# Kernel tuning notes

Hardware: AMD Instinct MI355X
Metric: run time of the kernel (lower is better)

Reference implementation:

```python
import jax, jax.numpy as jnp
import numpy as np

B, N, F_IN, T = 4, 512, 64, 16
K, F_CHEB, F_TIME, TS = 3, 64, 64, 1
E = 16384
LN_EPS = 1e-5


def setup_inputs() -> dict:
    key = jax.random.key(0)
    ks = jax.random.split(key, 18)
    s = 0.05
    X = jax.random.normal(ks[0], (B, N, F_IN, T), jnp.float32)
    # edges with guaranteed no self-loops (so remove_self_loops is a no-op)
    src = jax.random.randint(ks[1], (E,), 0, N, jnp.int32)
    off = jax.random.randint(ks[2], (E,), 1, N, jnp.int32)
    dst = (src + off) % N
    edge_index = jnp.stack([src, dst])
    return {
        'X': X,
        'edge_index': edge_index,
        'U1': jax.random.uniform(ks[3], (N,)) * s,
        'U2': jax.random.normal(ks[4], (F_IN, N)) * s,
        'U3': jax.random.uniform(ks[5], (F_IN,)) * s,
        'be': jax.random.normal(ks[6], (1, T, T)) * s,
        'Ve': jax.random.normal(ks[7], (T, T)) * s,
        'Ws1': jax.random.uniform(ks[8], (T,)) * s,
        'Ws2': jax.random.normal(ks[9], (F_IN, T)) * s,
        'Ws3': jax.random.uniform(ks[10], (F_IN,)) * s,
        'bs': jax.random.normal(ks[11], (1, N, N)) * s,
        'Vs': jax.random.normal(ks[12], (N, N)) * s,
        'W_cheb': jax.random.normal(ks[13], (K, F_IN, F_CHEB)) * s,
        'b_cheb': jax.random.uniform(ks[14], (F_CHEB,)) * s,
        'Wt': jax.random.normal(ks[15], (F_TIME, F_CHEB, 1, 3)) * s,
        'bt': jnp.zeros((F_TIME,), jnp.float32),
        'Wr': jax.random.normal(ks[16], (F_TIME, F_IN, 1, 1)) * s,
        'br': jnp.zeros((F_TIME,), jnp.float32),
        'gamma': jnp.ones((F_TIME,), jnp.float32),
        'beta': jnp.zeros((F_TIME,), jnp.float32),
    }


def _forward(edge_index, X, U1, U2, U3, be, Ve, Ws1, Ws2, Ws3, bs, Vs,
             W_cheb, b_cheb, Wt, bt, Wr, br, gamma, beta):
    Bn, Nn, Fn, Tn = X.shape
    # ---- temporal attention: (B,T,T)
    lhs_t = jnp.einsum('bnft,n->btf', X, U1) @ U2            # (B,T,N)
    rhs_t = jnp.einsum('f,bnft->bnt', U3, X)                 # (B,N,T)
    Et = jnp.matmul(Ve, jax.nn.sigmoid(jnp.matmul(lhs_t, rhs_t) + be))
    Et = jax.nn.softmax(Et, axis=1)
    # temporally re-weighted signal
    Xt = jnp.matmul(X.reshape(Bn, Nn * Fn, Tn), Et).reshape(Bn, Nn, Fn, Tn)
    # ---- spatial attention: (B,N,N)
    lhs_s = jnp.einsum('bnft,t->bnf', Xt, Ws1) @ Ws2         # (B,N,T)
    rhs_s = jnp.einsum('f,bnft->btn', Ws3, Xt)               # (B,T,N)
    S = jnp.matmul(Vs, jax.nn.sigmoid(jnp.matmul(lhs_s, rhs_s) + bs))
    S = jax.nn.softmax(S, axis=1)                            # (B,N,N)
    # ---- scaled sym-normalized Laplacian; lambda_max=2 so 2/lambda_max = 1.
    # edges: -D^-1/2 A D^-1/2 (E), +I self loops (N), then add_self_loops(-1) (N)
    row, col = edge_index[0], edge_index[1]
    ew = jnp.ones(row.shape, X.dtype)
    deg = jnp.zeros((Nn,), X.dtype).at[row].add(ew)
    dis = jnp.where(deg > 0, 1.0 / jnp.sqrt(jnp.maximum(deg, 1.0)), 0.0)  # deg is integral so max() only guards deg==0
    wn = -dis[row] * dis[col]
    loops = jnp.arange(Nn)
    rows = jnp.concatenate([row, loops, loops])
    cols = jnp.concatenate([col, loops, loops])
    norm = jnp.concatenate([wn, jnp.ones((Nn,), X.dtype), -jnp.ones((Nn,), X.dtype)])
    att_norm = norm[None, :] * S[:, rows, cols]              # (B,Etot)

    def prop(h, w):
        # propagate over transposed edges: gather at col, scatter-add at row
        # h: (B,T,N,F); w broadcastable to (B,1,Etot)
        msg = w[..., None] * h[:, :, cols, :]
        return jnp.zeros_like(h).at[:, :, rows, :].add(msg)

    xt = X.transpose(0, 3, 1, 2)                             # (B,T,N,F): ChebConv applied per timestep
    Tx0 = jnp.diagonal(S, axis1=1, axis2=2)[:, None, :, None] * xt  # diag(S) @ x
    out = jnp.einsum('btnf,fg->btng', Tx0, W_cheb[0])
    if W_cheb.shape[0] > 1:
        Tx1 = prop(Tx0, att_norm[:, None, :])
        out = out + jnp.einsum('btnf,fg->btng', Tx1, W_cheb[1])
    for k in range(2, W_cheb.shape[0]):
        Tx2 = 2.0 * prop(Tx1, norm[None, None, :]) - Tx0
        out = out + jnp.einsum('btnf,fg->btng', Tx2, W_cheb[k])
        Tx0, Tx1 = Tx1, Tx2
    X_hat = jax.nn.relu(out + b_cheb)                        # (B,T,N,Fc)
    # ---- time conv (1x3, stride (1,TS)) on (B,Fc,N,T) + residual 1x1 conv
    conv_t = jax.lax.conv_general_dilated(
        X_hat.transpose(0, 3, 2, 1), Wt, (1, TS), ((0, 0), (1, 1)),
        dimension_numbers=('NCHW', 'OIHW', 'NCHW')) + bt[None, :, None, None]
    conv_r = jax.lax.conv_general_dilated(
        X.transpose(0, 2, 1, 3), Wr, (1, TS), ((0, 0), (0, 0)),
        dimension_numbers=('NCHW', 'OIHW', 'NCHW')) + br[None, :, None, None]
    Z = jax.nn.relu(conv_r + conv_t).transpose(0, 3, 2, 1)   # (B,T,N,Ft)
    mu = jnp.mean(Z, -1, keepdims=True)
    var = jnp.var(Z, -1, keepdims=True)
    Z = (Z - mu) / jnp.sqrt(var + LN_EPS) * gamma + beta     # LayerNorm over Ft
    return Z.transpose(0, 2, 3, 1)                           # (B,N,Ft,T)


def reference(X, edge_index, U1, U2, U3, be, Ve, Ws1, Ws2, Ws3, bs, Vs,
              W_cheb, b_cheb, Wt, bt, Wr, br, gamma, beta):
    return _forward(edge_index, X, U1, U2, U3, be, Ve, Ws1, Ws2, Ws3, bs, Vs,
                    W_cheb, b_cheb, Wt, bt, Wr, br, gamma, beta)
```

## Files before the change

### kernel.cpp

```cpp
#include <hip/hip_runtime.h>
#include <math.h>

#define NB 4
#define NV 512
#define NF 64
#define NT 16
#define NE 16384

#define TX1_OFF    2097152u
#define SIGT_OFF   4194304u
#define XHAT_OFF   6291456u
#define ST_OFF     TX1_OFF
#define BST_OFF    8388608u
#define ET_OFF     8650752u
#define PART_OFF   8651776u
#define RHST_OFF   8684544u
#define LHSS_OFF   8717312u
#define RHSSN_OFF  8750080u
#define DIAGS_OFF  8782848u
#define CSRW_OFF   8850432u
#define WTT_OFF    8866816u
#define WRT_OFF    8879104u
#define RHS3_OFF   8883712u
#define EW1_OFF    8916480u
#define MPART_OFF  8916544u
#define FEND       8949312u

__global__ void k_prep(const int* __restrict__ ei, int* __restrict__ counts,
                       const float* __restrict__ Wt, const float* __restrict__ Wr,
                       const float* __restrict__ bs,
                       float* __restrict__ WtT, float* __restrict__ WrT,
                       float* __restrict__ bsT,
                       const float* __restrict__ X, const float* __restrict__ U1,
                       const float* __restrict__ U3, const float* __restrict__ Ws3,
                       float* __restrict__ part, float* __restrict__ rhs,
                       float* __restrict__ rhs3) {
    __shared__ int h[512];
    __shared__ float tile[64][65];
    int bid = blockIdx.x, tid = threadIdx.x;
    if (bid < 64) {
        int c = bid;
        h[tid] = 0; h[tid + 256] = 0;
        __syncthreads();
        atomicAdd(&h[ei[c * 256 + tid]], 1);
        __syncthreads();
        counts[c * 512 + tid] = h[tid];
        counts[c * 512 + tid + 256] = h[tid + 256];
    } else if (bid < 128) {
        int tb = bid - 64;
        int r0 = (tb >> 3) * 64, c0 = (tb & 7) * 64;
        int c = tid & 63, rq = tid >> 6;
        for (int k = 0; k < 16; ++k) {
            int r = rq * 16 + k;
            tile[r][c] = bs[(r0 + r) * 512 + c0 + c];
        }
        __syncthreads();
        int r2 = tid & 63;
        for (int k = 0; k < 16; ++k) {
            int c2 = rq * 16 + k;
            bsT[(size_t)(c0 + c2) * 512 + r0 + r2] = tile[r2][c2];
        }
    } else if (bid < 192) {
        int idx = (bid - 128) * 256 + tid;
        if (idx < 12288) {
            int o = idx & 63, gd = idx >> 6;
            int g = gd / 3, dt = gd - g * 3;
            WtT[idx] = Wt[(o * 64 + g) * 3 + dt];
        } else {
            int i2 = idx - 12288;
            int o = i2 & 63, f = i2 >> 6;
            WrT[i2] = Wr[o * 64 + f];
        }
    } else {
        int sub = bid - 192;
        if (sub < 32) {
            int b = sub >> 3, g = sub & 7;
            float acc[4] = {0.f, 0.f, 0.f, 0.f};
            const float* Xb = X + (size_t)b * NV * 1024;
            int n0 = g * 64;
            for (int nn = 0; nn < 64; ++nn) {
                int n = n0 + nn;
                float u = U1[n];
                const float* xp = Xb + (size_t)n * 1024;
#pragma unroll
                for (int k = 0; k < 4; ++k) acc[k] += xp[tid + 256 * k] * u;
            }
#pragma unroll
            for (int k = 0; k < 4; ++k) part[(size_t)(b * 8 + g) * 1024 + tid + 256 * k] = acc[k];
        } else {
            int gid = (sub - 32) * 256 + tid;
            int t = gid & 15;
            const float* xp = X + ((size_t)(gid >> 4)) * 1024 + t;
            float a = 0.f, a3 = 0.f;
#pragma unroll
            for (int f = 0; f < 64; ++f) {
                float v = xp[f * 16];
                a += U3[f] * v;
                a3 += Ws3[f] * v;
            }
            rhs[gid] = a;
            rhs3[gid] = a3;
        }
    }
}

__global__ __launch_bounds__(512) void k_fillscan(const int* __restrict__ ei,
                                                  const int* __restrict__ counts,
                                                  int* __restrict__ row_start,
                                                  int* __restrict__ csr_col,
                                                  float* __restrict__ csr_w) {
    __shared__ int sc[512];
    __shared__ int base_l[512];
    __shared__ float dis_l[512];
    __shared__ int rs_l[512];
    __shared__ int rowL[256];
    int c = blockIdx.x, tid = threadIdx.x;
    int r = tid;
    int sum = 0, base = 0;
    for (int cc = 0; cc < 64; ++cc) {
        if (cc == c) base = sum;
        sum += counts[cc * 512 + r];
    }
    base_l[r] = base;
    dis_l[r] = sum > 0 ? 1.0f / sqrtf((float)sum) : 0.0f;
    sc[r] = sum;
    __syncthreads();
    for (int off = 1; off < 512; off <<= 1) {
        int v = sc[r];
        int add = (r >= off) ? sc[r - off] : 0;
        __syncthreads();
        sc[r] = v + add;
        __syncthreads();
    }
    rs_l[r] = sc[r] - sum;
    if (c == 0) {
        row_start[r] = sc[r] - sum;
        if (r == 511) row_start[512] = sc[r];
    }
    if (tid < 256) rowL[tid] = ei[c * 256 + tid];
    __syncthreads();
    if (tid < 256) {
        int rr = rowL[tid];
        int col = ei[NE + c * 256 + tid];
        int rank = 0;
        for (int j = 0; j < tid; ++j)
            if (rowL[j] == rr) rank++;
        int pos = rs_l[rr] + base_l[rr] + rank;
        csr_col[pos] = col;
        csr_w[pos] = -dis_l[rr] * dis_l[col];
    }
}

__global__ void k_mpart(const float* __restrict__ rhs_g, const float* __restrict__ U2,
                        float* __restrict__ Mpart) {
    __shared__ float rhsL[1024];
    int b = blockIdx.x >> 3, g = blockIdx.x & 7;
    int tid = threadIdx.x;
#pragma unroll
    for (int k = 0; k < 4; ++k)
        rhsL[tid + 256 * k] = rhs_g[(size_t)b * 8192 + g * 1024 + tid + 256 * k];
    __syncthreads();
    float acc[4] = {0.f, 0.f, 0.f, 0.f};
    int fA[4], tA[4];
#pragma unroll
    for (int k = 0; k < 4; ++k) { int idx = tid + 256 * k; fA[k] = idx >> 4; tA[k] = idx & 15; }
    int n0 = g * 64;
    for (int nn = 0; nn < 64; ++nn) {
#pragma unroll
        for (int k = 0; k < 4; ++k)
            acc[k] += U2[fA[k] * 512 + n0 + nn] * rhsL[nn * 16 + tA[k]];
    }
#pragma unroll
    for (int k = 0; k < 4; ++k) Mpart[(size_t)(b * 8 + g) * 1024 + tid + 256 * k] = acc[k];
}

__global__ void k_temporal(const float* __restrict__ part, const float* __restrict__ Mpart,
                           const float* __restrict__ be,
                           const float* __restrict__ Ve, const float* __restrict__ Ws1,
                           float* __restrict__ Et, float* __restrict__ ew1) {
    __shared__ float lhs1[1024];
    __shared__ float M[1024];
    __shared__ float Esig[256];
    __shared__ float Et0[256];
    __shared__ float red[32];
    __shared__ float EtL[256];
    int b = blockIdx.x, tid = threadIdx.x;
#pragma unroll
    for (int k = 0; k < 4; ++k) {
        int idx = tid + 256 * k;
        float s = 0.f, m = 0.f;
        for (int g = 0; g < 8; ++g) {
            s += part[(size_t)(b * 8 + g) * 1024 + idx];
            m += Mpart[(size_t)(b * 8 + g) * 1024 + idx];
        }
        lhs1[idx] = s;
        M[idx] = m;
    }
    __syncthreads();
    {
        int t1 = tid >> 4, t2 = tid & 15;
        float s = 0.f;
        for (int f = 0; f < 64; ++f) s += lhs1[f * 16 + t1] * M[f * 16 + t2];
        s += be[t1 * 16 + t2];
        Esig[tid] = 1.f / (1.f + expf(-s));
    }
    __syncthreads();
    {
        int t1 = tid >> 4, t2 = tid & 15;
        float s = 0.f;
        for (int k = 0; k < 16; ++k) s += Ve[t1 * 16 + k] * Esig[k * 16 + t2];
        Et0[tid] = s;
    }
    __syncthreads();
    if (tid < 16) {
        float m = -1e30f;
        for (int k = 0; k < 16; ++k) m = fmaxf(m, Et0[k * 16 + tid]);
        float s = 0.f;
        for (int k = 0; k < 16; ++k) s += expf(Et0[k * 16 + tid] - m);
        red[tid] = m; red[16 + tid] = 1.f / s;
    }
    __syncthreads();
    {
        int t2 = tid & 15;
        float etv = expf(Et0[tid] - red[t2]) * red[16 + t2];
        Et[b * 256 + tid] = etv;
        EtL[tid] = etv;
    }
    __syncthreads();
    if (tid < 16) {
        float s = 0.f;
        for (int t = 0; t < 16; ++t) s += EtL[tid * 16 + t] * Ws1[t];
        ew1[b * 16 + tid] = s;
    }
}

__global__ __launch_bounds__(256) void k_spat2(const float* __restrict__ X,
                                               const float* __restrict__ ew1,
                                               const float* __restrict__ rhs3,
                                               const float* __restrict__ Et,
                                               const float* __restrict__ Ws2,
                                               float* __restrict__ lhs_s,
                                               float* __restrict__ rhs_sn) {
    int wv = threadIdx.x >> 6, lane = threadIdx.x & 63;
    int bn = blockIdx.x * 4 + wv;
    int b = bn >> 9;
    const float4* xp = (const float4*)(X + (size_t)bn * 1024 + lane * 16);
    float4 x0 = xp[0], x1 = xp[1], x2 = xp[2], x3 = xp[3];
    const float* e1 = ew1 + b * 16;
    float l1 = x0.x * e1[0] + x0.y * e1[1] + x0.z * e1[2] + x0.w * e1[3]
             + x1.x * e1[4] + x1.y * e1[5] + x1.z * e1[6] + x1.w * e1[7]
             + x2.x * e1[8] + x2.y * e1[9] + x2.z * e1[10] + x2.w * e1[11]
             + x3.x * e1[12] + x3.y * e1[13] + x3.z * e1[14] + x3.w * e1[15];
    const float4* wp = (const float4*)(Ws2 + lane * 16);
    float4 w0 = wp[0], w1 = wp[1], w2 = wp[2], w3 = wp[3];
    float p[16] = {l1 * w0.x, l1 * w0.y, l1 * w0.z, l1 * w0.w,
                   l1 * w1.x, l1 * w1.y, l1 * w1.z, l1 * w1.w,
                   l1 * w2.x, l1 * w2.y, l1 * w2.z, l1 * w2.w,
                   l1 * w3.x, l1 * w3.y, l1 * w3.z, l1 * w3.w};
#pragma unroll
    for (int off = 32; off; off >>= 1) {
#pragma unroll
        for (int k = 0; k < 16; ++k) p[k] += __shfl_xor(p[k], off);
    }
    if (lane == 0) {
        float4* lp = (float4*)(lhs_s + (size_t)bn * 16);
        lp[0] = make_float4(p[0], p[1], p[2], p[3]);
        lp[1] = make_float4(p[4], p[5], p[6], p[7]);
        lp[2] = make_float4(p[8], p[9], p[10], p[11]);
        lp[3] = make_float4(p[12], p[13], p[14], p[15]);
    }
    if (lane < 16) {
        const float* r3 = rhs3 + (size_t)bn * 16;
        const float* Eb = Et + b * 256;
        float s = 0.f;
#pragma unroll
        for (int tp = 0; tp < 16; ++tp) s += r3[tp] * Eb[tp * 16 + lane];
        rhs_sn[(size_t)bn * 16 + lane] = s;
    }
}

__global__ void k_sigT(const float* __restrict__ lhs_s, const float* __restrict__ rhs_sn,
                       const float* __restrict__ bsT, float* __restrict__ sigT) {
    int gid = blockIdx.x * 256 + threadIdx.x;
    int k = gid & 511, j = (gid >> 9) & 511, b = gid >> 18;
    const float4* lp = (const float4*)(lhs_s + (size_t)(b * 512 + k) * 16);
    const float4* rp = (const float4*)(rhs_sn + (size_t)(b * 512 + j) * 16);
    float s = 0.f;
#pragma unroll
    for (int q = 0; q < 4; ++q) {
        float4 a = lp[q], c = rp[q];
        s += a.x * c.x + a.y * c.y + a.z * c.z + a.w * c.w;
    }
    s += bsT[(size_t)j * 512 + k];
    sigT[gid] = 1.f / (1.f + expf(-s));
}

__global__ __launch_bounds__(256) void k_gemm_s(const float* __restrict__ sigT,
                                                const float* __restrict__ Vs,
                                                float* __restrict__ S0T) {
    __shared__ float As[32 * 68];
    __shared__ float Bs[32 * 68];
    int bI = blockIdx.x, bJ = blockIdx.y, b = blockIdx.z;
    int tid = threadIdx.x, tx = tid & 15, ty = tid >> 4;
    float acc[4][4] = {};
    const float* Ab = sigT + ((size_t)b * 512 + bJ * 64) * 512;
    const float* Bb = Vs + (size_t)bI * 64 * 512;
    for (int k0 = 0; k0 < 512; k0 += 32) {
#pragma unroll
        for (int p = 0; p < 2; ++p) {
            int idx = tid + 256 * p;
            int row = idx >> 3, kk = (idx & 7) * 4;
            float4 a = *(const float4*)(Ab + (size_t)row * 512 + k0 + kk);
            As[(kk + 0) * 68 + row] = a.x; As[(kk + 1) * 68 + row] = a.y;
            As[(kk + 2) * 68 + row] = a.z; As[(kk + 3) * 68 + row] = a.w;
            float4 v = *(const float4*)(Bb + (size_t)row * 512 + k0 + kk);
            Bs[(kk + 0) * 68 + row] = v.x; Bs[(kk + 1) * 68 + row] = v.y;
            Bs[(kk + 2) * 68 + row] = v.z; Bs[(kk + 3) * 68 + row] = v.w;
        }
        __syncthreads();
#pragma unroll
        for (int kk = 0; kk < 32; ++kk) {
            float4 a = *(const float4*)(As + kk * 68 + ty * 4);
            float4 bv = *(const float4*)(Bs + kk * 68 + tx * 4);
            acc[0][0] += a.x * bv.x; acc[0][1] += a.x * bv.y; acc[0][2] += a.x * bv.z; acc[0][3] += a.x * bv.w;
            acc[1][0] += a.y * bv.x; acc[1][1] += a.y * bv.y; acc[1][2] += a.y * bv.z; acc[1][3] += a.y * bv.w;
            acc[2][0] += a.z * bv.x; acc[2][1] += a.z * bv.y; acc[2][2] += a.z * bv.z; acc[2][3] += a.z * bv.w;
            acc[3][0] += a.w * bv.x; acc[3][1] += a.w * bv.y; acc[3][2] += a.w * bv.z; acc[3][3] += a.w * bv.w;
        }
        __syncthreads();
    }
    float* Cb = S0T + ((size_t)b * 512 + bJ * 64) * 512 + bI * 64;
#pragma unroll
    for (int y = 0; y < 4; ++y) {
        int j = ty * 4 + y;
        *(float4*)(Cb + (size_t)j * 512 + tx * 4) =
            make_float4(acc[y][0], acc[y][1], acc[y][2], acc[y][3]);
    }
}

__global__ void k_softmax_s(float* __restrict__ ST, float* __restrict__ diagS) {
    __shared__ float red[4];
    int bj = blockIdx.x;
    int b = bj >> 9, j = bj & 511;
    float* row = ST + (size_t)bj * 512;
    int tid = threadIdx.x;
    float v0 = row[tid], v1 = row[tid + 256];
    float m = fmaxf(v0, v1);
    for (int off = 32; off; off >>= 1) m = fmaxf(m, __shfl_xor(m, off));
    if ((tid & 63) == 0) red[tid >> 6] = m;
    __syncthreads();
    m = fmaxf(fmaxf(red[0], red[1]), fmaxf(red[2], red[3]));
    __syncthreads();
    float e0 = expf(v0 - m), e1 = expf(v1 - m);
    float s = e0 + e1;
    for (int off = 32; off; off >>= 1) s += __shfl_xor(s, off);
    if ((tid & 63) == 0) red[tid >> 6] = s;
    __syncthreads();
    s = red[0] + red[1] + red[2] + red[3];
    float inv = 1.f / s;
    float r0 = e0 * inv, r1 = e1 * inv;
    row[tid] = r0;
    row[tid + 256] = r1;
    if (j < 256) { if (tid == j) diagS[b * 512 + j] = r0; }
    else { if (tid == j - 256) diagS[b * 512 + j] = r1; }
}

__global__ __launch_bounds__(256) void k_prop1(const float* __restrict__ X,
                                               const float* __restrict__ ST,
                                               const float* __restrict__ diagS,
                                               const float* __restrict__ csr_w,
                                               const int* __restrict__ csr_col,
                                               const int* __restrict__ row_start,
                                               float* __restrict__ Tx1) {
    int blk = ((blockIdx.x & 7) << 8) + (blockIdx.x >> 3);
    int b = blk >> 9, i = blk & 511;
    int tid = threadIdx.x;
    int s = row_start[i], e2 = row_start[i + 1];
    const float4* Xb = (const float4*)(X + (size_t)b * 512 * 1024);
    const float* STb = ST + (size_t)b * 512 * 512;
    const float* dSb = diagS + b * 512;
    float4 acc = make_float4(0.f, 0.f, 0.f, 0.f);
    for (int p = s; p < e2; ++p) {
        int col = csr_col[p];
        float w = csr_w[p] * STb[(size_t)col * 512 + i] * dSb[col];
        float4 v = Xb[col * 256 + tid];
        acc.x += w * v.x; acc.y += w * v.y; acc.z += w * v.z; acc.w += w * v.w;
    }
    *(float4*)(Tx1 + (size_t)blk * 1024 + tid * 4) = acc;
}

__global__ __launch_bounds__(256) void k_pc(const float* __restrict__ X,
                                            const float* __restrict__ Tx1,
                                            const float* __restrict__ diagS,
                                            const float* __restrict__ csr_w,
                                            const int* __restrict__ csr_col,
                                            const int* __restrict__ row_start,
                                            const float* __restrict__ Wc,
                                            const float* __restrict__ bc,
                                            float* __restrict__ Xh) {
    __shared__ float t0s[1024], t1s[1024], t2s[1024];
    int blk = ((blockIdx.x & 7) << 8) + (blockIdx.x >> 3);
    int b = blk >> 9, i = blk & 511;
    int tid = threadIdx.x;
    int s = row_start[i], e2 = row_start[i + 1];
    const float* T1b = Tx1 + (size_t)b * 512 * 1024 + tid * 4;
    float4 acc = make_float4(0.f, 0.f, 0.f, 0.f);
    for (int p = s; p < e2; ++p) {
        int col = csr_col[p];
        float w = csr_w[p];
        float4 v = *(const float4*)(T1b + (size_t)col * 1024);
        acc.x += w * v.x; acc.y += w * v.y; acc.z += w * v.z; acc.w += w * v.w;
    }
    float ds = diagS[blk];
    size_t roff = (size_t)blk * 1024 + tid * 4;
    float4 x0 = *(const float4*)(X + roff);
    float4 t1v = *(const float4*)(Tx1 + roff);
    float4 t0v, t2v;
    t2v.x = 2.f * acc.x - ds * x0.x;
    t2v.y = 2.f * acc.y - ds * x0.y;
    t2v.z = 2.f * acc.z - ds * x0.z;
    t2v.w = 2.f * acc.w - ds * x0.w;
    t0v.x = x0.x * ds; t0v.y = x0.y * ds; t0v.z = x0.z * ds; t0v.w = x0.w * ds;
    *(float4*)(t0s + tid * 4) = t0v;
    *(float4*)(t1s + tid * 4) = t1v;
    *(float4*)(t2s + tid * 4) = t2v;
    __syncthreads();
    int g = tid >> 2, t4 = (tid & 3) * 4;
    float bcg = bc[g];
    float4 accg = make_float4(bcg, bcg, bcg, bcg);
    for (int f = 0; f < 64; ++f) {
        float w0 = Wc[f * 64 + g];
        float w1 = Wc[4096 + f * 64 + g];
        float w2 = Wc[8192 + f * 64 + g];
        float4 a0 = *(const float4*)(t0s + f * 16 + t4);
        float4 a1 = *(const float4*)(t1s + f * 16 + t4);
        float4 a2 = *(const float4*)(t2s + f * 16 + t4);
        accg.x += w0 * a0.x + w1 * a1.x + w2 * a2.x;
        accg.y += w0 * a0.y + w1 * a1.y + w2 * a2.y;
        accg.z += w0 * a0.z + w1 * a1.z + w2 * a2.z;
        accg.w += w0 * a0.w + w1 * a1.w + w2 * a2.w;
    }
    float4 o;
    o.x = fmaxf(accg.x, 0.f); o.y = fmaxf(accg.y, 0.f);
    o.z = fmaxf(accg.z, 0.f); o.w = fmaxf(accg.w, 0.f);
    *(float4*)(Xh + (size_t)blk * 1024 + g * 16 + t4) = o;
}

__global__ __launch_bounds__(256) void k_out(const float* __restrict__ X,
                                             const float* __restrict__ Xh,
                                             const float* __restrict__ WtT,
                                             const float* __restrict__ WrT,
                                             const float* __restrict__ bt,
                                             const float* __restrict__ br,
                                             const float* __restrict__ gamma,
                                             const float* __restrict__ beta,
                                             float* __restrict__ out) {
    __shared__ float xh[64 * 20];
    __shared__ float xl[64 * 16];
    __shared__ float red[4160];
    int bn = blockIdx.x;
    int tid = threadIdx.x;
    int o = tid & 63, q = tid >> 6;
    {
        int g = tid & 63, s4 = tid >> 6;
        int slot = (s4 == 0) ? 0 : 16 + s4;
        xh[g * 20 + slot] = 0.f;
    }
    {
        float4 v = ((const float4*)(Xh + (size_t)bn * 1024))[tid];
        int g = tid >> 2, t0 = (tid & 3) * 4;
        xh[g * 20 + t0 + 1] = v.x;
        xh[g * 20 + t0 + 2] = v.y;
        xh[g * 20 + t0 + 3] = v.z;
        xh[g * 20 + t0 + 4] = v.w;
        float4 u = ((const float4*)(X + (size_t)bn * 1024))[tid];
        *(float4*)(xl + tid * 4) = u;
    }
    __syncthreads();
    float acc[16];
#pragma unroll
    for (int k = 0; k < 16; ++k) acc[k] = 0.f;
    for (int gi = 0; gi < 16; ++gi) {
        int g = q * 16 + gi;
        const float4* xp = (const float4*)(xh + g * 20);
        float4 xa = xp[0], xb = xp[1], xc = xp[2], xd = xp[3], xe = xp[4];
        float xs[20] = {xa.x, xa.y, xa.z, xa.w, xb.x, xb.y, xb.z, xb.w,
                        xc.x, xc.y, xc.z, xc.w, xd.x, xd.y, xd.z, xd.w,
                        xe.x, xe.y, xe.z, xe.w};
        float w0 = WtT[(g * 3 + 0) * 64 + o];
        float w1 = WtT[(g * 3 + 1) * 64 + o];
        float w2 = WtT[(g * 3 + 2) * 64 + o];
#pragma unroll
        for (int tt = 0; tt < 16; ++tt)
            acc[tt] += xs[tt] * w0 + xs[tt + 1] * w1 + xs[tt + 2] * w2;
    }
    for (int fi = 0; fi < 16; ++fi) {
        int f = q * 16 + fi;
        const float4* xp = (const float4*)(xl + f * 16);
        float4 xa = xp[0], xb = xp[1], xc = xp[2], xd = xp[3];
        float xs[16] = {xa.x, xa.y, xa.z, xa.w, xb.x, xb.y, xb.z, xb.w,
                        xc.x, xc.y, xc.z, xc.w, xd.x, xd.y, xd.z, xd.w};
        float w = WrT[f * 64 + o];
#pragma unroll
        for (int tt = 0; tt < 16; ++tt) acc[tt] += xs[tt] * w;
    }
#pragma unroll
    for (int tt = 0; tt < 16; ++tt) red[q * 1024 + tt * 64 + o] = acc[tt];
    __syncthreads();
    float bsum = bt[o] + br[o];
    float go = gamma[o], bo = beta[o];
    float zv4[4];
#pragma unroll
    for (int tt = 0; tt < 4; ++tt) {
        int t = q * 4 + tt;
        float s = bsum;
#pragma unroll
        for (int qq = 0; qq < 4; ++qq) s += red[qq * 1024 + t * 64 + o];
        zv4[tt] = fmaxf(s, 0.f);
    }
    __syncthreads();
#pragma unroll
    for (int tt = 0; tt < 4; ++tt) {
        int t = q * 4 + tt;
        float zv = zv4[tt];
        float s = zv, sq = zv * zv;
        for (int off = 32; off; off >>= 1) {
            s += __shfl_xor(s, off);
            sq += __shfl_xor(sq, off);
        }
        float mu = s * (1.f / 64.f);
        float var = sq * (1.f / 64.f) - mu * mu;
        red[t * 65 + o] = (zv - mu) * rsqrtf(var + 1e-5f) * go + bo;
    }
    __syncthreads();
#pragma unroll
    for (int k = 0; k < 4; ++k) {
        int i = tid + 256 * k;
        out[(size_t)bn * 1024 + i] = red[(i & 15) * 65 + (i >> 4)];
    }
}

extern "C" void kernel_launch(void* const* d_in, const int* in_sizes, int n_in,
                              void* d_out, int out_size, void* d_ws, size_t ws_size,
                              hipStream_t stream) {
    const float* X     = (const float*)d_in[0];
    const int*   ei    = (const int*)d_in[1];
    const float* U1    = (const float*)d_in[2];
    const float* U2    = (const float*)d_in[3];
    const float* U3    = (const float*)d_in[4];
    const float* be    = (const float*)d_in[5];
    const float* Ve    = (const float*)d_in[6];
    const float* Ws1   = (const float*)d_in[7];
    const float* Ws2   = (const float*)d_in[8];
    const float* Ws3   = (const float*)d_in[9];
    const float* bs    = (const float*)d_in[10];
    const float* Vs    = (const float*)d_in[11];
    const float* Wc    = (const float*)d_in[12];
    const float* bc    = (const float*)d_in[13];
    const float* Wt    = (const float*)d_in[14];
    const float* bt    = (const float*)d_in[15];
    const float* Wr    = (const float*)d_in[16];
    const float* br    = (const float*)d_in[17];
    const float* gamma = (const float*)d_in[18];
    const float* beta  = (const float*)d_in[19];

    float* ws = (float*)d_ws;
    float* Tx1    = ws + TX1_OFF;
    float* Xh     = ws + XHAT_OFF;
    float* ST     = ws + ST_OFF;
    float* sigT   = ws + SIGT_OFF;
    float* bsT    = ws + BST_OFF;
    float* Et     = ws + ET_OFF;
    float* part   = ws + PART_OFF;
    float* rhs_t  = ws + RHST_OFF;
    float* lhs_s  = ws + LHSS_OFF;
    float* rhs_sn = ws + RHSSN_OFF;
    float* diagS  = ws + DIAGS_OFF;
    float* csr_w  = ws + CSRW_OFF;
    float* WtT    = ws + WTT_OFF;
    float* WrT    = ws + WRT_OFF;
    float* rhs3   = ws + RHS3_OFF;
    float* ew1    = ws + EW1_OFF;
    float* Mpart  = ws + MPART_OFF;

    int* ib        = (int*)(ws + FEND);
    int* row_start = ib;
    int* csr_col   = ib + 516;
    int* counts    = csr_col + NE;

    k_prep<<<352, 256, 0, stream>>>(ei, counts, Wt, Wr, bs, WtT, WrT, bsT,
                                    X, U1, U3, Ws3, part, rhs_t, rhs3);
    k_fillscan<<<64, 512, 0, stream>>>(ei, counts, row_start, csr_col, csr_w);

    k_mpart<<<32, 256, 0, stream>>>(rhs_t, U2, Mpart);
    k_temporal<<<4, 256, 0, stream>>>(part, Mpart, be, Ve, Ws1, Et, ew1);

    k_spat2<<<512, 256, 0, stream>>>(X, ew1, rhs3, Et, Ws2, lhs_s, rhs_sn);
    k_sigT<<<4096, 256, 0, stream>>>(lhs_s, rhs_sn, bsT, sigT);
    k_gemm_s<<<dim3(8, 8, 4), 256, 0, stream>>>(sigT, Vs, ST);
    k_softmax_s<<<2048, 256, 0, stream>>>(ST, diagS);

    k_prop1<<<2048, 256, 0, stream>>>(X, ST, diagS, csr_w, csr_col, row_start, Tx1);
    k_pc<<<2048, 256, 0, stream>>>(X, Tx1, diagS, csr_w, csr_col, row_start, Wc, bc, Xh);
    k_out<<<2048, 256, 0, stream>>>(X, Xh, WtT, WrT, bt, br, gamma, beta, (float*)d_out);
}
```

Before: 154.3 us.

## Fuse Chebyshev projection with output conv/LayerNorm and merge graph prep kernels

Merges the Chebyshev mixing kernel with the time-conv/residual/LayerNorm output kernel so X_hat stays in shared memory instead of a global intermediate. Also merges the CSR fill/scan kernel and the temporal Mpart partial GEMM into one launch with block-range dispatch. This cuts global traffic and launch count, at the cost of higher shared memory use per block and possible occupancy loss.

```diff
diff --git a/kernel.cpp b/kernel.cpp
--- a/kernel.cpp
+++ b/kernel.cpp
@@ -9,7 +9,6 @@
 
 #define TX1_OFF    2097152u
 #define SIGT_OFF   4194304u
-#define XHAT_OFF   6291456u
 #define ST_OFF     TX1_OFF
 #define BST_OFF    8388608u
 #define ET_OFF     8650752u
@@ -104,74 +103,76 @@
     }
 }
 
-__global__ __launch_bounds__(512) void k_fillscan(const int* __restrict__ ei,
-                                                  const int* __restrict__ counts,
-                                                  int* __restrict__ row_start,
-                                                  int* __restrict__ csr_col,
-                                                  float* __restrict__ csr_w) {
+__global__ __launch_bounds__(512) void k_graph(const int* __restrict__ ei,
+                                               const int* __restrict__ counts,
+                                               int* __restrict__ row_start,
+                                               int* __restrict__ csr_col,
+                                               float* __restrict__ csr_w,
+                                               const float* __restrict__ rhs_g,
+                                               const float* __restrict__ U2,
+                                               float* __restrict__ Mpart) {
     __shared__ int sc[512];
     __shared__ int base_l[512];
     __shared__ float dis_l[512];
     __shared__ int rs_l[512];
     __shared__ int rowL[256];
-    int c = blockIdx.x, tid = threadIdx.x;
-    int r = tid;
-    int sum = 0, base = 0;
-    for (int cc = 0; cc < 64; ++cc) {
-        if (cc == c) base = sum;
-        sum += counts[cc * 512 + r];
-    }
-    base_l[r] = base;
-    dis_l[r] = sum > 0 ? 1.0f / sqrtf((float)sum) : 0.0f;
-    sc[r] = sum;
-    __syncthreads();
-    for (int off = 1; off < 512; off <<= 1) {
-        int v = sc[r];
-        int add = (r >= off) ? sc[r - off] : 0;
-        __syncthreads();
-        sc[r] = v + add;
-        __syncthreads();
-    }
-    rs_l[r] = sc[r] - sum;
-    if (c == 0) {
-        row_start[r] = sc[r] - sum;
-        if (r == 511) row_start[512] = sc[r];
-    }
-    if (tid < 256) rowL[tid] = ei[c * 256 + tid];
-    __syncthreads();
-    if (tid < 256) {
-        int rr = rowL[tid];
-        int col = ei[NE + c * 256 + tid];
-        int rank = 0;
-        for (int j = 0; j < tid; ++j)
-            if (rowL[j] == rr) rank++;
-        int pos = rs_l[rr] + base_l[rr] + rank;
-        csr_col[pos] = col;
-        csr_w[pos] = -dis_l[rr] * dis_l[col];
-    }
-}
-
-__global__ void k_mpart(const float* __restrict__ rhs_g, const float* __restrict__ U2,
-                        float* __restrict__ Mpart) {
     __shared__ float rhsL[1024];
-    int b = blockIdx.x >> 3, g = blockIdx.x & 7;
-    int tid = threadIdx.x;
-#pragma unroll
-    for (int k = 0; k < 4; ++k)
-        rhsL[tid + 256 * k] = rhs_g[(size_t)b * 8192 + g * 1024 + tid + 256 * k];
-    __syncthreads();
-    float acc[4] = {0.f, 0.f, 0.f, 0.f};
-    int fA[4], tA[4];
-#pragma unroll
-    for (int k = 0; k < 4; ++k) { int idx = tid + 256 * k; fA[k] = idx >> 4; tA[k] = idx & 15; }
-    int n0 = g * 64;
-    for (int nn = 0; nn < 64; ++nn) {
-#pragma unroll
-        for (int k = 0; k < 4; ++k)
-            acc[k] += U2[fA[k] * 512 + n0 + nn] * rhsL[nn * 16 + tA[k]];
-    }
-#pragma unroll
-    for (int k = 0; k < 4; ++k) Mpart[(size_t)(b * 8 + g) * 1024 + tid + 256 * k] = acc[k];
+    int bid = blockIdx.x, tid = threadIdx.x;
+    if (bid < 64) {
+        int c = bid;
+        int r = tid;
+        int sum = 0, base = 0;
+        for (int cc = 0; cc < 64; ++cc) {
+            if (cc == c) base = sum;
+            sum += counts[cc * 512 + r];
+        }
+        base_l[r] = base;
+        dis_l[r] = sum > 0 ? 1.0f / sqrtf((float)sum) : 0.0f;
+        sc[r] = sum;
+        __syncthreads();
+        for (int off = 1; off < 512; off <<= 1) {
+            int v = sc[r];
+            int add = (r >= off) ? sc[r - off] : 0;
+            __syncthreads();
+            sc[r] = v + add;
+            __syncthreads();
+        }
+        rs_l[r] = sc[r] - sum;
+        if (c == 0) {
+            row_start[r] = sc[r] - sum;
+            if (r == 511) row_start[512] = sc[r];
+        }
+        if (tid < 256) rowL[tid] = ei[c * 256 + tid];
+        __syncthreads();
+        if (tid < 256) {
+            int rr = rowL[tid];
+            int col = ei[NE + c * 256 + tid];
+            int rank = 0;
+            for (int j = 0; j < tid; ++j)
+                if (rowL[j] == rr) rank++;
+            int pos = rs_l[rr] + base_l[rr] + rank;
+            csr_col[pos] = col;
+            csr_w[pos] = -dis_l[rr] * dis_l[col];
+        }
+    } else {
+        int sub = bid - 64;
+        int b = sub >> 3, g = sub & 7;
+        rhsL[tid] = rhs_g[(size_t)b * 8192 + g * 1024 + tid];
+        rhsL[tid + 512] = rhs_g[(size_t)b * 8192 + g * 1024 + tid + 512];
+        __syncthreads();
+        float acc[2] = {0.f, 0.f};
+        int fA[2], tA[2];
+#pragma unroll
+        for (int k = 0; k < 2; ++k) { int idx = tid + 512 * k; fA[k] = idx >> 4; tA[k] = idx & 15; }
+        int n0 = g * 64;
+        for (int nn = 0; nn < 64; ++nn) {
+#pragma unroll
+            for (int k = 0; k < 2; ++k)
+                acc[k] += U2[fA[k] * 512 + n0 + nn] * rhsL[nn * 16 + tA[k]];
+        }
+#pragma unroll
+        for (int k = 0; k < 2; ++k) Mpart[(size_t)(b * 8 + g) * 1024 + tid + 512 * k] = acc[k];
+    }
 }
 
 __global__ void k_temporal(const float* __restrict__ part, const float* __restrict__ Mpart,
@@ -389,19 +390,29 @@
     *(float4*)(Tx1 + (size_t)blk * 1024 + tid * 4) = acc;
 }
 
-__global__ __launch_bounds__(256) void k_pc(const float* __restrict__ X,
-                                            const float* __restrict__ Tx1,
-                                            const float* __restrict__ diagS,
-                                            const float* __restrict__ csr_w,
-                                            const int* __restrict__ csr_col,
-                                            const int* __restrict__ row_start,
-                                            const float* __restrict__ Wc,
-                                            const float* __restrict__ bc,
-                                            float* __restrict__ Xh) {
-    __shared__ float t0s[1024], t1s[1024], t2s[1024];
+__global__ __launch_bounds__(256) void k_pco(const float* __restrict__ X,
+                                             const float* __restrict__ Tx1,
+                                             const float* __restrict__ diagS,
+                                             const float* __restrict__ csr_w,
+                                             const int* __restrict__ csr_col,
+                                             const int* __restrict__ row_start,
+                                             const float* __restrict__ Wc,
+                                             const float* __restrict__ bc,
+                                             const float* __restrict__ WtT,
+                                             const float* __restrict__ WrT,
+                                             const float* __restrict__ bt,
+                                             const float* __restrict__ br,
+                                             const float* __restrict__ gamma,
+                                             const float* __restrict__ beta,
+                                             float* __restrict__ out) {
+    __shared__ float buf[4160];
+    __shared__ float xl[1024];
+    __shared__ float xh[1280];
     int blk = ((blockIdx.x & 7) << 8) + (blockIdx.x >> 3);
     int b = blk >> 9, i = blk & 511;
     int tid = threadIdx.x;
+#pragma unroll
+    for (int k = 0; k < 5; ++k) xh[tid + 256 * k] = 0.f;
     int s = row_start[i], e2 = row_start[i + 1];
     const float* T1b = Tx1 + (size_t)b * 512 * 1024 + tid * 4;
     float4 acc = make_float4(0.f, 0.f, 0.f, 0.f);
@@ -421,65 +432,41 @@
     t2v.z = 2.f * acc.z - ds * x0.z;
     t2v.w = 2.f * acc.w - ds * x0.w;
     t0v.x = x0.x * ds; t0v.y = x0.y * ds; t0v.z = x0.z * ds; t0v.w = x0.w * ds;
-    *(float4*)(t0s + tid * 4) = t0v;
-    *(float4*)(t1s + tid * 4) = t1v;
-    *(float4*)(t2s + tid * 4) = t2v;
-    __syncthreads();
-    int g = tid >> 2, t4 = (tid & 3) * 4;
-    float bcg = bc[g];
-    float4 accg = make_float4(bcg, bcg, bcg, bcg);
-    for (int f = 0; f < 64; ++f) {
-        float w0 = Wc[f * 64 + g];
-        float w1 = Wc[4096 + f * 64 + g];
-        float w2 = Wc[8192 + f * 64 + g];
-        float4 a0 = *(const float4*)(t0s + f * 16 + t4);
-        float4 a1 = *(const float4*)(t1s + f * 16 + t4);
-        float4 a2 = *(const float4*)(t2s + f * 16 + t4);
-        accg.x += w0 * a0.x + w1 * a1.x + w2 * a2.x;
-        accg.y += w0 * a0.y + w1 * a1.y + w2 * a2.y;
-        accg.z += w0 * a0.z + w1 * a1.z + w2 * a2.z;
-        accg.w += w0 * a0.w + w1 * a1.w + w2 * a2.w;
-    }
-    float4 o;
-    o.x = fmaxf(accg.x, 0.f); o.y = fmaxf(accg.y, 0.f);
-    o.z = fmaxf(accg.z, 0.f); o.w = fmaxf(accg.w, 0.f);
-    *(float4*)(Xh + (size_t)blk * 1024 + g * 16 + t4) = o;
-}
-
-__global__ __launch_bounds__(256) void k_out(const float* __restrict__ X,
-                                             const float* __restrict__ Xh,
-                                             const float* __restrict__ WtT,
-                                             const float* __restrict__ WrT,
-                                             const float* __restrict__ bt,
-                                             const float* __restrict__ br,
-                                             const float* __restrict__ gamma,
-                                             const float* __restrict__ beta,
-                                             float* __restrict__ out) {
-    __shared__ float xh[64 * 20];
-    __shared__ float xl[64 * 16];
-    __shared__ float red[4160];
-    int bn = blockIdx.x;
-    int tid = threadIdx.x;
+    *(float4*)(buf + tid * 4) = t0v;
+    *(float4*)(buf + 1024 + tid * 4) = t1v;
+    *(float4*)(buf + 2048 + tid * 4) = t2v;
+    *(float4*)(xl + tid * 4) = x0;
+    __syncthreads();
+    {
+        int g = tid >> 2, t4 = (tid & 3) * 4;
+        float bcg = bc[g];
+        float4 accg = make_float4(bcg, bcg, bcg, bcg);
+        const float* t0s = buf;
+        const float* t1s = buf + 1024;
+        const float* t2s = buf + 2048;
+        for (int f = 0; f < 64; ++f) {
+            float w0 = Wc[f * 64 + g];
+            float w1 = Wc[4096 + f * 64 + g];
+            float w2 = Wc[8192 + f * 64 + g];
+            float4 a0 = *(const float4*)(t0s + f * 16 + t4);
+            float4 a1 = *(const float4*)(t1s + f * 16 + t4);
+            float4 a2 = *(const float4*)(t2s + f * 16 + t4);
+            accg.x += w0 * a0.x + w1 * a1.x + w2 * a2.x;
+            accg.y += w0 * a0.y + w1 * a1.y + w2 * a2.y;
+            accg.z += w0 * a0.z + w1 * a1.z + w2 * a2.z;
+            accg.w += w0 * a0.w + w1 * a1.w + w2 * a2.w;
+        }
+        xh[g * 20 + t4 + 1] = fmaxf(accg.x, 0.f);
+        xh[g * 20 + t4 + 2] = fmaxf(accg.y, 0.f);
+        xh[g * 20 + t4 + 3] = fmaxf(accg.z, 0.f);
+        xh[g * 20 + t4 + 4] = fmaxf(accg.w, 0.f);
+    }
+    __syncthreads();
+    float* red = buf;
     int o = tid & 63, q = tid >> 6;
-    {
-        int g = tid & 63, s4 = tid >> 6;
-        int slot = (s4 == 0) ? 0 : 16 + s4;
-        xh[g * 20 + slot] = 0.f;
-    }
-    {
-        float4 v = ((const float4*)(Xh + (size_t)bn * 1024))[tid];
-        int g = tid >> 2, t0 = (tid & 3) * 4;
-        xh[g * 20 + t0 + 1] = v.x;
-        xh[g * 20 + t0 + 2] = v.y;
-        xh[g * 20 + t0 + 3] = v.z;
-        xh[g * 20 + t0 + 4] = v.w;
-        float4 u = ((const float4*)(X + (size_t)bn * 1024))[tid];
-        *(float4*)(xl + tid * 4) = u;
-    }
-    __syncthreads();
-    float acc[16];
-#pragma unroll
-    for (int k = 0; k < 16; ++k) acc[k] = 0.f;
+    float accv[16];
+#pragma unroll
+    for (int k = 0; k < 16; ++k) accv[k] = 0.f;
     for (int gi = 0; gi < 16; ++gi) {
         int g = q * 16 + gi;
         const float4* xp = (const float4*)(xh + g * 20);
@@ -492,7 +479,7 @@
         float w2 = WtT[(g * 3 + 2) * 64 + o];
 #pragma unroll
         for (int tt = 0; tt < 16; ++tt)
-            acc[tt] += xs[tt] * w0 + xs[tt + 1] * w1 + xs[tt + 2] * w2;
+            accv[tt] += xs[tt] * w0 + xs[tt + 1] * w1 + xs[tt + 2] * w2;
     }
     for (int fi = 0; fi < 16; ++fi) {
         int f = q * 16 + fi;
@@ -502,10 +489,10 @@
                         xc.x, xc.y, xc.z, xc.w, xd.x, xd.y, xd.z, xd.w};
         float w = WrT[f * 64 + o];
 #pragma unroll
-        for (int tt = 0; tt < 16; ++tt) acc[tt] += xs[tt] * w;
-    }
-#pragma unroll
-    for (int tt = 0; tt < 16; ++tt) red[q * 1024 + tt * 64 + o] = acc[tt];
+        for (int tt = 0; tt < 16; ++tt) accv[tt] += xs[tt] * w;
+    }
+#pragma unroll
+    for (int tt = 0; tt < 16; ++tt) red[q * 1024 + tt * 64 + o] = accv[tt];
     __syncthreads();
     float bsum = bt[o] + br[o];
     float go = gamma[o], bo = beta[o];
@@ -513,30 +500,30 @@
 #pragma unroll
     for (int tt = 0; tt < 4; ++tt) {
         int t = q * 4 + tt;
-        float s = bsum;
-#pragma unroll
-        for (int qq = 0; qq < 4; ++qq) s += red[qq * 1024 + t * 64 + o];
-        zv4[tt] = fmaxf(s, 0.f);
+        float sv = bsum;
+#pragma unroll
+        for (int qq = 0; qq < 4; ++qq) sv += red[qq * 1024 + t * 64 + o];
+        zv4[tt] = fmaxf(sv, 0.f);
     }
     __syncthreads();
 #pragma unroll
     for (int tt = 0; tt < 4; ++tt) {
         int t = q * 4 + tt;
         float zv = zv4[tt];
-        float s = zv, sq = zv * zv;
+        float sv = zv, sq = zv * zv;
         for (int off = 32; off; off >>= 1) {
-            s += __shfl_xor(s, off);
+            sv += __shfl_xor(sv, off);
             sq += __shfl_xor(sq, off);
         }
-        float mu = s * (1.f / 64.f);
+        float mu = sv * (1.f / 64.f);
         float var = sq * (1.f / 64.f) - mu * mu;
         red[t * 65 + o] = (zv - mu) * rsqrtf(var + 1e-5f) * go + bo;
     }
     __syncthreads();
 #pragma unroll
     for (int k = 0; k < 4; ++k) {
-        int i = tid + 256 * k;
-        out[(size_t)bn * 1024 + i] = red[(i & 15) * 65 + (i >> 4)];
+        int idx = tid + 256 * k;
+        out[(size_t)blk * 1024 + idx] = red[(idx & 15) * 65 + (idx >> 4)];
     }
 }
 
@@ -566,7 +553,6 @@
 
     float* ws = (float*)d_ws;
     float* Tx1    = ws + TX1_OFF;
-    float* Xh     = ws + XHAT_OFF;
     float* ST     = ws + ST_OFF;
     float* sigT   = ws + SIGT_OFF;
     float* bsT    = ws + BST_OFF;
@@ -590,9 +576,9 @@
 
     k_prep<<<352, 256, 0, stream>>>(ei, counts, Wt, Wr, bs, WtT, WrT, bsT,
                                     X, U1, U3, Ws3, part, rhs_t, rhs3);
-    k_fillscan<<<64, 512, 0, stream>>>(ei, counts, row_start, csr_col, csr_w);
-
-    k_mpart<<<32, 256, 0, stream>>>(rhs_t, U2, Mpart);
+    k_graph<<<96, 512, 0, stream>>>(ei, counts, row_start, csr_col, csr_w,
+                                    rhs_t, U2, Mpart);
+
     k_temporal<<<4, 256, 0, stream>>>(part, Mpart, be, Ve, Ws1, Et, ew1);
 
     k_spat2<<<512, 256, 0, stream>>>(X, ew1, rhs3, Et, Ws2, lhs_s, rhs_sn);
@@ -601,6 +587,7 @@
     k_softmax_s<<<2048, 256, 0, stream>>>(ST, diagS);
 
     k_prop1<<<2048, 256, 0, stream>>>(X, ST, diagS, csr_w, csr_col, row_start, Tx1);
-    k_pc<<<2048, 256, 0, stream>>>(X, Tx1, diagS, csr_w, csr_col, row_start, Wc, bc, Xh);
-    k_out<<<2048, 256, 0, stream>>>(X, Xh, WtT, WrT, bt, br, gamma, beta, (float*)d_out);
-}
+    k_pco<<<2048, 256, 0, stream>>>(X, Tx1, diagS, csr_w, csr_col, row_start,
+                                    Wc, bc, WtT, WrT, bt, br, gamma, beta,
+                                    (float*)d_out);
+}
```

Result: faster. 146.7 us (-4.9%).
